# Performance work log

Hardware: AMD Instinct MI355X
Metric: run time of the kernel (lower is better)

Reference implementation:

```python
import jax, jax.numpy as jnp
import numpy as np

N = 400000
INC = 32
OUTC = 32
K = 27  # 3x3x3 kernel offsets
BN_EPS = 1e-5


def setup_inputs() -> dict:
    key = jax.random.key(0)
    ks = jax.random.split(key, 6)
    feats = jax.random.normal(ks[0], (N, INC), dtype=jnp.float32)
    kernel = jax.random.normal(ks[1], (K, INC, OUTC), dtype=jnp.float32) * 0.05
    bn_gamma = jnp.ones((OUTC,), dtype=jnp.float32)
    bn_beta = jnp.zeros((OUTC,), dtype=jnp.float32)
    bn_mean = jax.random.normal(ks[2], (OUTC,), dtype=jnp.float32) * 0.1
    bn_var = jax.random.uniform(ks[3], (OUTC,), dtype=jnp.float32) + 0.5
    in_idx = jax.random.randint(ks[4], (K, N), 0, N, dtype=jnp.int32)
    out_idx = jax.random.randint(ks[5], (K, N), 0, N, dtype=jnp.int32)
    return {"feats": feats, "kernel": kernel, "bn_gamma": bn_gamma,
            "bn_beta": bn_beta, "bn_mean": bn_mean, "bn_var": bn_var,
            "in_idx": in_idx, "out_idx": out_idx}


def _sparse_conv(feats, kernel, in_idx, out_idx):
    # gather -> per-offset matmul -> scatter-add, looped over the 27 offsets
    # via lax.scan to avoid materializing a [K, N, C] intermediate.
    out0 = jnp.zeros((feats.shape[0], kernel.shape[-1]), dtype=feats.dtype)

    def step(out, xs):
        w_k, iin, iout = xs  # [inc,outc], [M], [M]
        gathered = feats[iin]              # [M, inc]  irregular gather
        contrib = gathered @ w_k           # [M, outc] per-offset GEMM
        return out.at[iout].add(contrib), None  # scatter-accumulate

    out, _ = jax.lax.scan(step, out0, (kernel, in_idx, out_idx))
    return out


def reference(feats, kernel, bn_gamma, bn_beta, bn_mean, bn_var, in_idx, out_idx):
    out = _sparse_conv(feats, kernel, in_idx, out_idx)
    # BatchNorm (eval mode, running stats) over the feature dim
    inv_std = jax.lax.rsqrt(bn_var + BN_EPS)
    out = (out - bn_mean) * (bn_gamma * inv_std) + bn_beta
    # ReLU
    return jnp.maximum(out, 0.0)
```

## Files before the change

### kernel.cpp

```cpp
#include <hip/hip_runtime.h>
#include <hip/hip_bf16.h>
#include <hip/hip_fp16.h>

constexpr int INC  = 32;
constexpr int OUTC = 32;
constexpr int CHROWS  = 256;
constexpr int NSLICE  = 8;
constexpr int CAPB    = 384;
constexpr int CPS_MAX = 208;
constexpr int ACCW    = 17;

typedef __bf16 bf16x8 __attribute__((ext_vector_type(8)));
typedef float  f32x4  __attribute__((ext_vector_type(4)));
typedef __attribute__((address_space(3))) unsigned long long lds_u64;


__device__ __forceinline__ void lds_add_u64(unsigned long long* p,
                                            unsigned long long v) {
    __hip_atomic_fetch_add((lds_u64*)p, v,
                           __ATOMIC_RELAXED, __HIP_MEMORY_SCOPE_WORKGROUP);
}

__device__ __forceinline__ unsigned long long enc2(float a, float b) {
    const int q0 = __float2int_rn(fminf(fmaxf(a, -8.f), 8.f) * 65536.0f);
    const int q1 = __float2int_rn(fminf(fmaxf(b, -8.f), 8.f) * 65536.0f);
    return (unsigned long long)((long long)q0 + ((long long)q1 << 32));
}

__global__ __launch_bounds__(256) void prep_feats(
    const float* __restrict__ f, __bf16* __restrict__ fb, int total8)
{
    int i = blockIdx.x * 256 + threadIdx.x;
    const int stride = gridDim.x * 256;
    for (; i < total8; i += stride) {
        const float4* p = (const float4*)(f + (size_t)i * 8);
        const float4 a = p[0], b = p[1];
        bf16x8 v;
        v[0] = (__bf16)a.x; v[1] = (__bf16)a.y; v[2] = (__bf16)a.z; v[3] = (__bf16)a.w;
        v[4] = (__bf16)b.x; v[5] = (__bf16)b.y; v[6] = (__bf16)b.z; v[7] = (__bf16)b.w;
        *(bf16x8*)(fb + (size_t)i * 8) = v;
    }
}

__global__ __launch_bounds__(1024) void fill_chunks(
    const int* __restrict__ in_idx,
    const int* __restrict__ out_idx,
    unsigned* __restrict__ recsB,
    unsigned* __restrict__ cntB,
    int N, int cps, int slice_rows)
{
    __shared__ unsigned cur[CPS_MAX];
    const int s = blockIdx.x, k = blockIdx.y;
    const int tid = threadIdx.x;
    for (int c = tid; c < cps; c += 1024) cur[c] = 0u;
    __syncthreads();

    const int* iin_p  = in_idx  + (size_t)k * N;
    const int* iout_p = out_idx + (size_t)k * N;
    const int nchunkpad = NSLICE * cps;
    const unsigned lo = (unsigned)(s * slice_rows);
    const unsigned hi = lo + (unsigned)slice_rows;
    const size_t segbase = ((size_t)k * nchunkpad + (size_t)s * cps) * CAPB;

    for (int i0 = tid * 4; i0 < N; i0 += 4096) {
        const int4 ov = *(const int4*)(iout_p + i0);
        const int4 iv = *(const int4*)(iin_p + i0);
        const unsigned o[4]  = {(unsigned)ov.x, (unsigned)ov.y,
                                (unsigned)ov.z, (unsigned)ov.w};
        const unsigned ii[4] = {(unsigned)iv.x, (unsigned)iv.y,
                                (unsigned)iv.z, (unsigned)iv.w};
#pragma unroll
        for (int j = 0; j < 4; ++j) {
            if (o[j] >= lo && o[j] < hi) {
                const unsigned olo  = o[j] - lo;
                const unsigned c    = olo >> 8;
                const unsigned lrow = olo & 255u;
                const unsigned pos = atomicAdd(&cur[c], 1u);
                if (pos < (unsigned)CAPB)
                    recsB[segbase + (size_t)c * CAPB + pos] = ii[j] | (lrow << 19);
            }
        }
    }
    __syncthreads();
    for (int c = tid; c < cps; c += 1024)
        cntB[(size_t)k * nchunkpad + (size_t)s * cps + c] =
            min(cur[c], (unsigned)CAPB);
}

template<bool BF16F>
__global__ __launch_bounds__(576) void conv_chunk(
    const float*  __restrict__ feats,
    const __bf16* __restrict__ fbf,
    const float*  __restrict__ wkern,
    const unsigned* __restrict__ recsB,
    const unsigned* __restrict__ cntB,
    const float* __restrict__ gamma, const float* __restrict__ beta,
    const float* __restrict__ mean,  const float* __restrict__ var,
    float* __restrict__ out, int N, int nchunkpad)
{
    __shared__ unsigned long long accw[(CHROWS + 1) * ACCW];
    const int tid = threadIdx.x;
    for (int i = tid; i < (CHROWS + 1) * ACCW; i += 576) accw[i] = 0ull;
    __syncthreads();

    const int c    = blockIdx.x;
    const int wid  = tid >> 6;
    const int lane = tid & 63;
    const int col  = lane & 15;
    const int quad = lane >> 4;

#pragma unroll
    for (int kk = 0; kk < 3; ++kk) {
        const int k = wid + kk * 9;
        const int bidx = k * nchunkpad + c;
        const int cnt = (int)cntB[bidx];
        if (cnt == 0) continue;
        const unsigned* seg = recsB + (size_t)bidx * CAPB;

        const float* wk = wkern + (size_t)k * (INC * OUTC);
        bf16x8 b0, b1;
#pragma unroll
        for (int j = 0; j < 8; ++j) {
            const float2 w2 = *(const float2*)(wk + (quad * 8 + j) * OUTC + 2 * col);
            b0[j] = (__bf16)w2.x;
            b1[j] = (__bf16)w2.y;
        }

        const int ntile = (cnt + 15) >> 4;

        auto do_tile = [&](int t) {
            const int sbase = t << 4;
            const unsigned ra = seg[sbase + col];
            const unsigned iidx = (sbase + col < cnt) ? (ra & 0x7FFFFu) : 0u;
            bf16x8 a;
            if constexpr (BF16F) {
                a = *(const bf16x8*)(fbf + (size_t)iidx * INC + quad * 8);
            } else {
                const float4* ap = (const float4*)(feats + (size_t)iidx * INC + quad * 8);
                const float4 alo = ap[0], ahi = ap[1];
                a[0] = (__bf16)alo.x; a[1] = (__bf16)alo.y;
                a[2] = (__bf16)alo.z; a[3] = (__bf16)alo.w;
                a[4] = (__bf16)ahi.x; a[5] = (__bf16)ahi.y;
                a[6] = (__bf16)ahi.z; a[7] = (__bf16)ahi.w;
            }
            const uint4 rv = *(const uint4*)(seg + sbase + quad * 4);
            f32x4 acc0 = {0.f, 0.f, 0.f, 0.f};
            f32x4 acc1 = {0.f, 0.f, 0.f, 0.f};
            acc0 = __builtin_amdgcn_mfma_f32_16x16x32_bf16(a, b0, acc0, 0, 0, 0);
            acc1 = __builtin_amdgcn_mfma_f32_16x16x32_bf16(a, b1, acc1, 0, 0, 0);
            const unsigned rr[4] = { rv.x, rv.y, rv.z, rv.w };
#pragma unroll
            for (int r = 0; r < 4; ++r) {
                const int idx  = sbase + quad * 4 + r;
                const int lrow = (idx < cnt) ? (int)((rr[r] >> 19) & 255u) : CHROWS;
                lds_add_u64(&accw[lrow * ACCW + col], enc2(acc0[r], acc1[r]));
            }
        };

        int t = 0;
        for (; t + 2 <= ntile; t += 2) {
            const int s0 = t << 4, s1 = s0 + 16;
            const unsigned ra0 = seg[s0 + col];
            const unsigned ra1 = seg[s1 + col];
            const uint4 rv0 = *(const uint4*)(seg + s0 + quad * 4);
            const uint4 rv1 = *(const uint4*)(seg + s1 + quad * 4);
            const unsigned i0 = (s0 + col < cnt) ? (ra0 & 0x7FFFFu) : 0u;
            const unsigned i1 = (s1 + col < cnt) ? (ra1 & 0x7FFFFu) : 0u;

            bf16x8 a0, a1;
            if constexpr (BF16F) {
                a0 = *(const bf16x8*)(fbf + (size_t)i0 * INC + quad * 8);
                a1 = *(const bf16x8*)(fbf + (size_t)i1 * INC + quad * 8);
            } else {
                const float4* p0 = (const float4*)(feats + (size_t)i0 * INC + quad * 8);
                const float4* p1 = (const float4*)(feats + (size_t)i1 * INC + quad * 8);
                const float4 a0lo = p0[0], a0hi = p0[1];
                const float4 a1lo = p1[0], a1hi = p1[1];
                a0[0] = (__bf16)a0lo.x; a0[1] = (__bf16)a0lo.y;
                a0[2] = (__bf16)a0lo.z; a0[3] = (__bf16)a0lo.w;
                a0[4] = (__bf16)a0hi.x; a0[5] = (__bf16)a0hi.y;
                a0[6] = (__bf16)a0hi.z; a0[7] = (__bf16)a0hi.w;
                a1[0] = (__bf16)a1lo.x; a1[1] = (__bf16)a1lo.y;
                a1[2] = (__bf16)a1lo.z; a1[3] = (__bf16)a1lo.w;
                a1[4] = (__bf16)a1hi.x; a1[5] = (__bf16)a1hi.y;
                a1[6] = (__bf16)a1hi.z; a1[7] = (__bf16)a1hi.w;
            }

            f32x4 c00 = {0.f, 0.f, 0.f, 0.f};
            f32x4 c01 = {0.f, 0.f, 0.f, 0.f};
            f32x4 c10 = {0.f, 0.f, 0.f, 0.f};
            f32x4 c11 = {0.f, 0.f, 0.f, 0.f};
            c00 = __builtin_amdgcn_mfma_f32_16x16x32_bf16(a0, b0, c00, 0, 0, 0);
            c01 = __builtin_amdgcn_mfma_f32_16x16x32_bf16(a0, b1, c01, 0, 0, 0);
            c10 = __builtin_amdgcn_mfma_f32_16x16x32_bf16(a1, b0, c10, 0, 0, 0);
            c11 = __builtin_amdgcn_mfma_f32_16x16x32_bf16(a1, b1, c11, 0, 0, 0);

            const unsigned rr0[4] = { rv0.x, rv0.y, rv0.z, rv0.w };
            const unsigned rr1[4] = { rv1.x, rv1.y, rv1.z, rv1.w };
#pragma unroll
            for (int r = 0; r < 4; ++r) {
                const int idx0  = s0 + quad * 4 + r;
                const int lrow0 = (idx0 < cnt) ? (int)((rr0[r] >> 19) & 255u) : CHROWS;
                lds_add_u64(&accw[lrow0 * ACCW + col], enc2(c00[r], c01[r]));
            }
#pragma unroll
            for (int r = 0; r < 4; ++r) {
                const int idx1  = s1 + quad * 4 + r;
                const int lrow1 = (idx1 < cnt) ? (int)((rr1[r] >> 19) & 255u) : CHROWS;
                lds_add_u64(&accw[lrow1 * ACCW + col], enc2(c10[r], c11[r]));
            }
        }
        for (; t < ntile; ++t) do_tile(t);
    }
    __syncthreads();

    if (tid < 512) {
        const int p  = tid & 15;
        const int c0 = 2 * p;
        const int r0 = tid >> 4;
        const float s0 = gamma[c0]     * rsqrtf(var[c0]     + 1e-5f);
        const float s1 = gamma[c0 + 1] * rsqrtf(var[c0 + 1] + 1e-5f);
        const float q0 = beta[c0]     - mean[c0]     * s0;
        const float q1 = beta[c0 + 1] - mean[c0 + 1] * s1;
#pragma unroll
        for (int it = 0; it < CHROWS / 32; ++it) {
            const int row  = it * 32 + r0;
            const int grow = c * CHROWS + row;
            if (grow < N) {
                long long t = (long long)accw[row * ACCW + p];
                const int d0 = (int)(unsigned)(t & 0xFFFFFFFFll);
                const int d1 = (int)((t - (long long)d0) >> 32);
                float2 o;
                o.x = fmaxf(fmaf((float)d0 * (1.f / 65536.f), s0, q0), 0.f);
                o.y = fmaxf(fmaf((float)d1 * (1.f / 65536.f), s1, q1), 0.f);
                *(float2*)(out + (size_t)grow * OUTC + c0) = o;
            }
        }
    }
}

__global__ __launch_bounds__(256) void scatter_conv_mfma_pk(
    const float* __restrict__ feats,
    const float* __restrict__ wkern,
    const int*   __restrict__ in_idx,
    const int*   __restrict__ out_idx,
    __half2*     __restrict__ ws,
    int N)
{
    const int k    = blockIdx.y;
    const int lane = threadIdx.x & 63;
    const int col  = lane & 15;
    const int quad = lane >> 4;

    const int wave   = blockIdx.x * 4 + (threadIdx.x >> 6);
    const int nwaves = gridDim.x * 4;

    const float* wk = wkern + (size_t)k * (INC * OUTC);
    bf16x8 b0, b1;
#pragma unroll
    for (int j = 0; j < 8; ++j) {
        const int kk = quad * 8 + j;
        b0[j] = (__bf16)wk[kk * OUTC + 2 * col];
        b1[j] = (__bf16)wk[kk * OUTC + 2 * col + 1];
    }

    const int* iin_p  = in_idx  + (size_t)k * N;
    const int* iout_p = out_idx + (size_t)k * N;
    const int  ntiles = N >> 4;

    for (int t = wave; t < ntiles; t += nwaves) {
        const int base = t << 4;
        const int iin = iin_p[base + col];
        int orow[4];
#pragma unroll
        for (int r = 0; r < 4; ++r) orow[r] = iout_p[base + quad * 4 + r];

        const float4* ap = (const float4*)(feats + (size_t)iin * INC + quad * 8);
        const float4 a_lo = ap[0];
        const float4 a_hi = ap[1];
        bf16x8 a;
        a[0] = (__bf16)a_lo.x; a[1] = (__bf16)a_lo.y;
        a[2] = (__bf16)a_lo.z; a[3] = (__bf16)a_lo.w;
        a[4] = (__bf16)a_hi.x; a[5] = (__bf16)a_hi.y;
        a[6] = (__bf16)a_hi.z; a[7] = (__bf16)a_hi.w;

        f32x4 acc0 = {0.f, 0.f, 0.f, 0.f};
        f32x4 acc1 = {0.f, 0.f, 0.f, 0.f};
        acc0 = __builtin_amdgcn_mfma_f32_16x16x32_bf16(a, b0, acc0, 0, 0, 0);
        acc1 = __builtin_amdgcn_mfma_f32_16x16x32_bf16(a, b1, acc1, 0, 0, 0);

#pragma unroll
        for (int r = 0; r < 4; ++r) {
            __half2 v = __halves2half2(__float2half(acc0[r]), __float2half(acc1[r]));
            unsafeAtomicAdd(ws + (size_t)orow[r] * 16 + col, v);
        }
    }
}

__global__ __launch_bounds__(256) void bn_relu_f16(
    const __half2* __restrict__ ws,
    float* __restrict__ out,
    const float* __restrict__ gamma,
    const float* __restrict__ beta,
    const float* __restrict__ mean,
    const float* __restrict__ var,
    int total2)
{
    const int tid    = blockIdx.x * blockDim.x + threadIdx.x;
    const int stride = gridDim.x * blockDim.x;
    const int p      = tid & 15;
    const int c0     = 2 * p;

    float s0 = gamma[c0]     * rsqrtf(var[c0]     + 1e-5f);
    float s1 = gamma[c0 + 1] * rsqrtf(var[c0 + 1] + 1e-5f);
    float q0 = beta[c0]     - mean[c0]     * s0;
    float q1 = beta[c0 + 1] - mean[c0 + 1] * s1;

    float2* po = (float2*)out;
    for (int i = tid; i < total2; i += stride) {
        const __half2 h = ws[i];
        float2 v;
        v.x = fmaxf(fmaf(__low2float(h),  s0, q0), 0.0f);
        v.y = fmaxf(fmaf(__high2float(h), s1, q1), 0.0f);
        po[i] = v;
    }
}

__global__ __launch_bounds__(256) void scatter_conv_mfma_f32(
    const float* __restrict__ feats,
    const float* __restrict__ wkern,
    const int*   __restrict__ in_idx,
    const int*   __restrict__ out_idx,
    float*       __restrict__ out,
    int N)
{
    const int k    = blockIdx.y;
    const int lane = threadIdx.x & 63;
    const int col  = lane & 15;
    const int quad = lane >> 4;
    const int wave   = blockIdx.x * 4 + (threadIdx.x >> 6);
    const int nwaves = gridDim.x * 4;

    const float* wk = wkern + (size_t)k * (INC * OUTC);
    bf16x8 b0, b1;
#pragma unroll
    for (int j = 0; j < 8; ++j) {
        const int kk = quad * 8 + j;
        b0[j] = (__bf16)wk[kk * OUTC + col];
        b1[j] = (__bf16)wk[kk * OUTC + 16 + col];
    }

    const int* iin_p  = in_idx  + (size_t)k * N;
    const int* iout_p = out_idx + (size_t)k * N;
    const int  ntiles = N >> 4;

    for (int t = wave; t < ntiles; t += nwaves) {
        const int base = t << 4;
        const int iin = iin_p[base + col];
        int orow[4];
#pragma unroll
        for (int r = 0; r < 4; ++r) orow[r] = iout_p[base + quad * 4 + r];

        const float4* ap = (const float4*)(feats + (size_t)iin * INC + quad * 8);
        const float4 a_lo = ap[0];
        const float4 a_hi = ap[1];
        bf16x8 a;
        a[0] = (__bf16)a_lo.x; a[1] = (__bf16)a_lo.y;
        a[2] = (__bf16)a_lo.z; a[3] = (__bf16)a_lo.w;
        a[4] = (__bf16)a_hi.x; a[5] = (__bf16)a_hi.y;
        a[6] = (__bf16)a_hi.z; a[7] = (__bf16)a_hi.w;

        f32x4 acc0 = {0.f, 0.f, 0.f, 0.f};
        f32x4 acc1 = {0.f, 0.f, 0.f, 0.f};
        acc0 = __builtin_amdgcn_mfma_f32_16x16x32_bf16(a, b0, acc0, 0, 0, 0);
        acc1 = __builtin_amdgcn_mfma_f32_16x16x32_bf16(a, b1, acc1, 0, 0, 0);

#pragma unroll
        for (int r = 0; r < 4; ++r) {
            float* dst = out + (size_t)orow[r] * OUTC + col;
            unsafeAtomicAdd(dst,      acc0[r]);
            unsafeAtomicAdd(dst + 16, acc1[r]);
        }
    }
}

__global__ __launch_bounds__(256) void bn_relu_f32_inplace(
    float* __restrict__ out,
    const float* __restrict__ gamma,
    const float* __restrict__ beta,
    const float* __restrict__ mean,
    const float* __restrict__ var,
    int total4)
{
    const int tid    = blockIdx.x * blockDim.x + threadIdx.x;
    const int stride = gridDim.x * blockDim.x;
    const int c0     = (tid & 7) << 2;

    float s[4], b[4];
#pragma unroll
    for (int j = 0; j < 4; ++j) {
        const int c = c0 + j;
        s[j] = gamma[c] * rsqrtf(var[c] + 1e-5f);
        b[j] = beta[c] - mean[c] * s[j];
    }

    float4* p = (float4*)out;
    for (int i = tid; i < total4; i += stride) {
        float4 v = p[i];
        v.x = fmaxf(fmaf(v.x, s[0], b[0]), 0.0f);
        v.y = fmaxf(fmaf(v.y, s[1], b[1]), 0.0f);
        v.z = fmaxf(fmaf(v.z, s[2], b[2]), 0.0f);
        v.w = fmaxf(fmaf(v.w, s[3], b[3]), 0.0f);
        p[i] = v;
    }
}

extern "C" void kernel_launch(void* const* d_in, const int* in_sizes, int n_in,
                              void* d_out, int out_size, void* d_ws, size_t ws_size,
                              hipStream_t stream) {
    const float* feats   = (const float*)d_in[0];
    const float* wkern   = (const float*)d_in[1];
    const float* gamma   = (const float*)d_in[2];
    const float* beta    = (const float*)d_in[3];
    const float* mean    = (const float*)d_in[4];
    const float* var     = (const float*)d_in[5];
    const int*   in_idx  = (const int*)d_in[6];
    const int*   out_idx = (const int*)d_in[7];
    float*       out     = (float*)d_out;

    const int N = in_sizes[0] / INC;
    const int K = in_sizes[1] / (INC * OUTC);

    const int nchunk     = (N + CHROWS - 1) / CHROWS;
    const int cps        = (nchunk + NSLICE - 1) / NSLICE;
    const int nchunkpad  = NSLICE * cps;
    const int slice_rows = cps * CHROWS;

    auto al = [](size_t x) { return (x + 255) & ~(size_t)255; };
    size_t off = 0;
    const size_t cntB_off  = off; off = al(off + (size_t)K * nchunkpad * 4);
    const size_t recsB_off = off; off = al(off + (size_t)K * nchunkpad * CAPB * 4);
    const size_t need_core = off;
    const size_t fbf_off   = off;
    const size_t need_full = off + al((size_t)N * INC * 2);
    const size_t need_pk   = (size_t)N * OUTC * sizeof(__half);

    const bool chunk_ok = (N <= (1 << 19)) && (N % 4 == 0) &&
                          (cps <= CPS_MAX) && (K == 27);

    if (chunk_ok && ws_size >= need_core) {
        char* base = (char*)d_ws;
        unsigned* cntB  = (unsigned*)(base + cntB_off);
        unsigned* recsB = (unsigned*)(base + recsB_off);

        const bool use_bf16 = ws_size >= need_full;
        if (use_bf16) {
            __bf16* fbf = (__bf16*)(base + fbf_off);
            prep_feats<<<768, 256, 0, stream>>>(feats, fbf, N * 4);
            fill_chunks<<<dim3(NSLICE, K), 1024, 0, stream>>>(
                in_idx, out_idx, recsB, cntB, N, cps, slice_rows);
            conv_chunk<true><<<nchunk, 576, 0, stream>>>(
                feats, fbf, wkern, recsB, cntB, gamma, beta, mean, var,
                out, N, nchunkpad);
        } else {
            fill_chunks<<<dim3(NSLICE, K), 1024, 0, stream>>>(
                in_idx, out_idx, recsB, cntB, N, cps, slice_rows);
            conv_chunk<false><<<nchunk, 576, 0, stream>>>(
                feats, nullptr, wkern, recsB, cntB, gamma, beta, mean, var,
                out, N, nchunkpad);
        }
    } else if (ws_size >= need_pk) {
        __half2* acc = (__half2*)d_ws;
        hipMemsetAsync(acc, 0, need_pk, stream);
        dim3 grid(80, K);
        scatter_conv_mfma_pk<<<grid, 256, 0, stream>>>(
            feats, wkern, in_idx, out_idx, acc, N);
        bn_relu_f16<<<1024, 256, 0, stream>>>(acc, out, gamma, beta, mean, var, N * 16);
    } else {
        hipMemsetAsync(out, 0, (size_t)out_size * sizeof(float), stream);
        dim3 grid(80, K);
        scatter_conv_mfma_f32<<<grid, 256, 0, stream>>>(
            feats, wkern, in_idx, out_idx, out, N);
        bn_relu_f32_inplace<<<1024, 256, 0, stream>>>(
            out, gamma, beta, mean, var, out_size / 4);
    }
}
```

Measured before the change: 559.6 us.

## Partition index scan across blocks and bin records per chunk-part

```diff
diff --git a/kernel.cpp b/kernel.cpp
--- a/kernel.cpp
+++ b/kernel.cpp
@@ -4,15 +4,16 @@
 
 constexpr int INC  = 32;
 constexpr int OUTC = 32;
-constexpr int CHROWS  = 256;
-constexpr int NSLICE  = 8;
-constexpr int CAPB    = 384;
-constexpr int CPS_MAX = 208;
-constexpr int ACCW    = 17;
+constexpr int CHROWS = 256;
+constexpr int NPART  = 8;
+constexpr int CAPP   = 80;
+constexpr int NCHMAX = 2048;
+constexpr int ACCW   = 17;
 
 typedef __bf16 bf16x8 __attribute__((ext_vector_type(8)));
 typedef float  f32x4  __attribute__((ext_vector_type(4)));
 typedef __attribute__((address_space(3))) unsigned long long lds_u64;
+typedef __attribute__((address_space(3))) unsigned           lds_u32;
 
 
 __device__ __forceinline__ void lds_add_u64(unsigned long long* p,
@@ -20,10 +21,14 @@
     __hip_atomic_fetch_add((lds_u64*)p, v,
                            __ATOMIC_RELAXED, __HIP_MEMORY_SCOPE_WORKGROUP);
 }
+__device__ __forceinline__ unsigned lds_add_u32(unsigned* p, unsigned v) {
+    return __hip_atomic_fetch_add((lds_u32*)p, v,
+                                  __ATOMIC_RELAXED, __HIP_MEMORY_SCOPE_WORKGROUP);
+}
 
 __device__ __forceinline__ unsigned long long enc2(float a, float b) {
-    const int q0 = __float2int_rn(fminf(fmaxf(a, -8.f), 8.f) * 65536.0f);
-    const int q1 = __float2int_rn(fminf(fmaxf(b, -8.f), 8.f) * 65536.0f);
+    const int q0 = __float2int_rn(a * 65536.0f);
+    const int q1 = __float2int_rn(b * 65536.0f);
     return (unsigned long long)((long long)q0 + ((long long)q1 << 32));
 }
 
@@ -42,27 +47,27 @@
     }
 }
 
-__global__ __launch_bounds__(1024) void fill_chunks(
+__global__ __launch_bounds__(1024) void fill_parts(
     const int* __restrict__ in_idx,
     const int* __restrict__ out_idx,
     unsigned* __restrict__ recsB,
     unsigned* __restrict__ cntB,
-    int N, int cps, int slice_rows)
-{
-    __shared__ unsigned cur[CPS_MAX];
-    const int s = blockIdx.x, k = blockIdx.y;
+    int N, int nchunk, int nchunkpad)
+{
+    __shared__ unsigned cur[NCHMAX];
+    const int p = blockIdx.x, k = blockIdx.y;
     const int tid = threadIdx.x;
-    for (int c = tid; c < cps; c += 1024) cur[c] = 0u;
+    for (int c = tid; c < nchunk; c += 1024) cur[c] = 0u;
     __syncthreads();
 
+    const int part_n  = N / NPART;
+    const int ibeg    = p * part_n;
+    const int iend    = ibeg + part_n;
     const int* iin_p  = in_idx  + (size_t)k * N;
     const int* iout_p = out_idx + (size_t)k * N;
-    const int nchunkpad = NSLICE * cps;
-    const unsigned lo = (unsigned)(s * slice_rows);
-    const unsigned hi = lo + (unsigned)slice_rows;
-    const size_t segbase = ((size_t)k * nchunkpad + (size_t)s * cps) * CAPB;
-
-    for (int i0 = tid * 4; i0 < N; i0 += 4096) {
+    const size_t kbase8 = (size_t)k * nchunkpad * NPART;
+
+    for (int i0 = ibeg + tid * 4; i0 < iend; i0 += 4096) {
         const int4 ov = *(const int4*)(iout_p + i0);
         const int4 iv = *(const int4*)(iin_p + i0);
         const unsigned o[4]  = {(unsigned)ov.x, (unsigned)ov.y,
@@ -71,20 +76,17 @@
                                 (unsigned)iv.z, (unsigned)iv.w};
 #pragma unroll
         for (int j = 0; j < 4; ++j) {
-            if (o[j] >= lo && o[j] < hi) {
-                const unsigned olo  = o[j] - lo;
-                const unsigned c    = olo >> 8;
-                const unsigned lrow = olo & 255u;
-                const unsigned pos = atomicAdd(&cur[c], 1u);
-                if (pos < (unsigned)CAPB)
-                    recsB[segbase + (size_t)c * CAPB + pos] = ii[j] | (lrow << 19);
-            }
+            const unsigned c    = o[j] >> 8;
+            const unsigned lrow = o[j] & 255u;
+            const unsigned pos  = lds_add_u32(&cur[c], 1u);
+            if (pos < (unsigned)CAPP)
+                recsB[(kbase8 + (size_t)c * NPART + p) * CAPP + pos]
+                    = ii[j] | (lrow << 19);
         }
     }
     __syncthreads();
-    for (int c = tid; c < cps; c += 1024)
-        cntB[(size_t)k * nchunkpad + (size_t)s * cps + c] =
-            min(cur[c], (unsigned)CAPB);
+    for (int c = tid; c < nchunk; c += 1024)
+        cntB[kbase8 + (size_t)c * NPART + p] = min(cur[c], (unsigned)CAPP);
 }
 
 template<bool BF16F>
@@ -109,13 +111,10 @@
     const int col  = lane & 15;
     const int quad = lane >> 4;
 
-#pragma unroll
+#pragma unroll 1
     for (int kk = 0; kk < 3; ++kk) {
         const int k = wid + kk * 9;
-        const int bidx = k * nchunkpad + c;
-        const int cnt = (int)cntB[bidx];
-        if (cnt == 0) continue;
-        const unsigned* seg = recsB + (size_t)bidx * CAPB;
+        const size_t bidx8 = ((size_t)k * nchunkpad + c) * NPART;
 
         const float* wk = wkern + (size_t)k * (INC * OUTC);
         bf16x8 b0, b1;
@@ -126,91 +125,97 @@
             b1[j] = (__bf16)w2.y;
         }
 
-        const int ntile = (cnt + 15) >> 4;
-
-        auto do_tile = [&](int t) {
-            const int sbase = t << 4;
-            const unsigned ra = seg[sbase + col];
-            const unsigned iidx = (sbase + col < cnt) ? (ra & 0x7FFFFu) : 0u;
-            bf16x8 a;
-            if constexpr (BF16F) {
-                a = *(const bf16x8*)(fbf + (size_t)iidx * INC + quad * 8);
-            } else {
-                const float4* ap = (const float4*)(feats + (size_t)iidx * INC + quad * 8);
-                const float4 alo = ap[0], ahi = ap[1];
-                a[0] = (__bf16)alo.x; a[1] = (__bf16)alo.y;
-                a[2] = (__bf16)alo.z; a[3] = (__bf16)alo.w;
-                a[4] = (__bf16)ahi.x; a[5] = (__bf16)ahi.y;
-                a[6] = (__bf16)ahi.z; a[7] = (__bf16)ahi.w;
+#pragma unroll 1
+        for (int p = 0; p < NPART; ++p) {
+            const int cnt = (int)cntB[bidx8 + p];
+            if (cnt == 0) continue;
+            const unsigned* seg = recsB + (bidx8 + p) * CAPP;
+            const int ntile = (cnt + 15) >> 4;
+
+            auto do_tile = [&](int t) {
+                const int sbase = t << 4;
+                const unsigned ra = seg[sbase + col];
+                const unsigned iidx = (sbase + col < cnt) ? (ra & 0x7FFFFu) : 0u;
+                bf16x8 a;
+                if constexpr (BF16F) {
+                    a = *(const bf16x8*)(fbf + (size_t)iidx * INC + quad * 8);
+                } else {
+                    const float4* ap = (const float4*)(feats + (size_t)iidx * INC + quad * 8);
+                    const float4 alo = ap[0], ahi = ap[1];
+                    a[0] = (__bf16)alo.x; a[1] = (__bf16)alo.y;
+                    a[2] = (__bf16)alo.z; a[3] = (__bf16)alo.w;
+                    a[4] = (__bf16)ahi.x; a[5] = (__bf16)ahi.y;
+                    a[6] = (__bf16)ahi.z; a[7] = (__bf16)ahi.w;
+                }
+                const uint4 rv = *(const uint4*)(seg + sbase + quad * 4);
+                f32x4 acc0 = {0.f, 0.f, 0.f, 0.f};
+                f32x4 acc1 = {0.f, 0.f, 0.f, 0.f};
+                acc0 = __builtin_amdgcn_mfma_f32_16x16x32_bf16(a, b0, acc0, 0, 0, 0);
+                acc1 = __builtin_amdgcn_mfma_f32_16x16x32_bf16(a, b1, acc1, 0, 0, 0);
+                const unsigned rr[4] = { rv.x, rv.y, rv.z, rv.w };
+#pragma unroll
+                for (int r = 0; r < 4; ++r) {
+                    const int idx  = sbase + quad * 4 + r;
+                    const int lrow = (idx < cnt) ? (int)((rr[r] >> 19) & 255u) : CHROWS;
+                    lds_add_u64(&accw[lrow * ACCW + col], enc2(acc0[r], acc1[r]));
+                }
+            };
+
+            int t = 0;
+            for (; t + 2 <= ntile; t += 2) {
+                const int s0 = (t << 4), s1 = s0 + 16;
+                const unsigned ra0 = seg[s0 + col];
+                const unsigned ra1 = seg[s1 + col];
+                const uint4 rv0 = *(const uint4*)(seg + s0 + quad * 4);
+                const uint4 rv1 = *(const uint4*)(seg + s1 + quad * 4);
+                const unsigned i0 = (s0 + col < cnt) ? (ra0 & 0x7FFFFu) : 0u;
+                const unsigned i1 = (s1 + col < cnt) ? (ra1 & 0x7FFFFu) : 0u;
+
+                bf16x8 a0, a1;
+                if constexpr (BF16F) {
+                    a0 = *(const bf16x8*)(fbf + (size_t)i0 * INC + quad * 8);
+                    a1 = *(const bf16x8*)(fbf + (size_t)i1 * INC + quad * 8);
+                } else {
+                    const float4* p0 = (const float4*)(feats + (size_t)i0 * INC + quad * 8);
+                    const float4* p1 = (const float4*)(feats + (size_t)i1 * INC + quad * 8);
+                    const float4 a0lo = p0[0], a0hi = p0[1];
+                    const float4 a1lo = p1[0], a1hi = p1[1];
+                    a0[0] = (__bf16)a0lo.x; a0[1] = (__bf16)a0lo.y;
+                    a0[2] = (__bf16)a0lo.z; a0[3] = (__bf16)a0lo.w;
+                    a0[4] = (__bf16)a0hi.x; a0[5] = (__bf16)a0hi.y;
+                    a0[6] = (__bf16)a0hi.z; a0[7] = (__bf16)a0hi.w;
+                    a1[0] = (__bf16)a1lo.x; a1[1] = (__bf16)a1lo.y;
+                    a1[2] = (__bf16)a1lo.z; a1[3] = (__bf16)a1lo.w;
+                    a1[4] = (__bf16)a1hi.x; a1[5] = (__bf16)a1hi.y;
+                    a1[6] = (__bf16)a1hi.z; a1[7] = (__bf16)a1hi.w;
+                }
+
+                f32x4 c00 = {0.f, 0.f, 0.f, 0.f};
+                f32x4 c01 = {0.f, 0.f, 0.f, 0.f};
+                f32x4 c10 = {0.f, 0.f, 0.f, 0.f};
+                f32x4 c11 = {0.f, 0.f, 0.f, 0.f};
+                c00 = __builtin_amdgcn_mfma_f32_16x16x32_bf16(a0, b0, c00, 0, 0, 0);
+                c01 = __builtin_amdgcn_mfma_f32_16x16x32_bf16(a0, b1, c01, 0, 0, 0);
+                c10 = __builtin_amdgcn_mfma_f32_16x16x32_bf16(a1, b0, c10, 0, 0, 0);
+                c11 = __builtin_amdgcn_mfma_f32_16x16x32_bf16(a1, b1, c11, 0, 0, 0);
+
+                const unsigned rr0[4] = { rv0.x, rv0.y, rv0.z, rv0.w };
+                const unsigned rr1[4] = { rv1.x, rv1.y, rv1.z, rv1.w };
+#pragma unroll
+                for (int r = 0; r < 4; ++r) {
+                    const int idx0  = s0 + quad * 4 + r;
+                    const int lrow0 = (idx0 < cnt) ? (int)((rr0[r] >> 19) & 255u) : CHROWS;
+                    lds_add_u64(&accw[lrow0 * ACCW + col], enc2(c00[r], c01[r]));
+                }
+#pragma unroll
+                for (int r = 0; r < 4; ++r) {
+                    const int idx1  = s1 + quad * 4 + r;
+                    const int lrow1 = (idx1 < cnt) ? (int)((rr1[r] >> 19) & 255u) : CHROWS;
+                    lds_add_u64(&accw[lrow1 * ACCW + col], enc2(c10[r], c11[r]));
+                }
             }
-            const uint4 rv = *(const uint4*)(seg + sbase + quad * 4);
-            f32x4 acc0 = {0.f, 0.f, 0.f, 0.f};
-            f32x4 acc1 = {0.f, 0.f, 0.f, 0.f};
-            acc0 = __builtin_amdgcn_mfma_f32_16x16x32_bf16(a, b0, acc0, 0, 0, 0);
-            acc1 = __builtin_amdgcn_mfma_f32_16x16x32_bf16(a, b1, acc1, 0, 0, 0);
-            const unsigned rr[4] = { rv.x, rv.y, rv.z, rv.w };
-#pragma unroll
-            for (int r = 0; r < 4; ++r) {
-                const int idx  = sbase + quad * 4 + r;
-                const int lrow = (idx < cnt) ? (int)((rr[r] >> 19) & 255u) : CHROWS;
-                lds_add_u64(&accw[lrow * ACCW + col], enc2(acc0[r], acc1[r]));
-            }
-        };
-
-        int t = 0;
-        for (; t + 2 <= ntile; t += 2) {
-            const int s0 = t << 4, s1 = s0 + 16;
-            const unsigned ra0 = seg[s0 + col];
-            const unsigned ra1 = seg[s1 + col];
-            const uint4 rv0 = *(const uint4*)(seg + s0 + quad * 4);
-            const uint4 rv1 = *(const uint4*)(seg + s1 + quad * 4);
-            const unsigned i0 = (s0 + col < cnt) ? (ra0 & 0x7FFFFu) : 0u;
-            const unsigned i1 = (s1 + col < cnt) ? (ra1 & 0x7FFFFu) : 0u;
-
-            bf16x8 a0, a1;
-            if constexpr (BF16F) {
-                a0 = *(const bf16x8*)(fbf + (size_t)i0 * INC + quad * 8);
-                a1 = *(const bf16x8*)(fbf + (size_t)i1 * INC + quad * 8);
-            } else {
-                const float4* p0 = (const float4*)(feats + (size_t)i0 * INC + quad * 8);
-                const float4* p1 = (const float4*)(feats + (size_t)i1 * INC + quad * 8);
-                const float4 a0lo = p0[0], a0hi = p0[1];
-                const float4 a1lo = p1[0], a1hi = p1[1];
-                a0[0] = (__bf16)a0lo.x; a0[1] = (__bf16)a0lo.y;
-                a0[2] = (__bf16)a0lo.z; a0[3] = (__bf16)a0lo.w;
-                a0[4] = (__bf16)a0hi.x; a0[5] = (__bf16)a0hi.y;
-                a0[6] = (__bf16)a0hi.z; a0[7] = (__bf16)a0hi.w;
-                a1[0] = (__bf16)a1lo.x; a1[1] = (__bf16)a1lo.y;
-                a1[2] = (__bf16)a1lo.z; a1[3] = (__bf16)a1lo.w;
-                a1[4] = (__bf16)a1hi.x; a1[5] = (__bf16)a1hi.y;
-                a1[6] = (__bf16)a1hi.z; a1[7] = (__bf16)a1hi.w;
-            }
-
-            f32x4 c00 = {0.f, 0.f, 0.f, 0.f};
-            f32x4 c01 = {0.f, 0.f, 0.f, 0.f};
-            f32x4 c10 = {0.f, 0.f, 0.f, 0.f};
-            f32x4 c11 = {0.f, 0.f, 0.f, 0.f};
-            c00 = __builtin_amdgcn_mfma_f32_16x16x32_bf16(a0, b0, c00, 0, 0, 0);
-            c01 = __builtin_amdgcn_mfma_f32_16x16x32_bf16(a0, b1, c01, 0, 0, 0);
-            c10 = __builtin_amdgcn_mfma_f32_16x16x32_bf16(a1, b0, c10, 0, 0, 0);
-            c11 = __builtin_amdgcn_mfma_f32_16x16x32_bf16(a1, b1, c11, 0, 0, 0);
-
-            const unsigned rr0[4] = { rv0.x, rv0.y, rv0.z, rv0.w };
-            const unsigned rr1[4] = { rv1.x, rv1.y, rv1.z, rv1.w };
-#pragma unroll
-            for (int r = 0; r < 4; ++r) {
-                const int idx0  = s0 + quad * 4 + r;
-                const int lrow0 = (idx0 < cnt) ? (int)((rr0[r] >> 19) & 255u) : CHROWS;
-                lds_add_u64(&accw[lrow0 * ACCW + col], enc2(c00[r], c01[r]));
-            }
-#pragma unroll
-            for (int r = 0; r < 4; ++r) {
-                const int idx1  = s1 + quad * 4 + r;
-                const int lrow1 = (idx1 < cnt) ? (int)((rr1[r] >> 19) & 255u) : CHROWS;
-                lds_add_u64(&accw[lrow1 * ACCW + col], enc2(c10[r], c11[r]));
-            }
-        }
-        for (; t < ntile; ++t) do_tile(t);
+            for (; t < ntile; ++t) do_tile(t);
+        }
     }
     __syncthreads();
 
@@ -431,22 +436,22 @@
     const int N = in_sizes[0] / INC;
     const int K = in_sizes[1] / (INC * OUTC);
 
-    const int nchunk     = (N + CHROWS - 1) / CHROWS;
-    const int cps        = (nchunk + NSLICE - 1) / NSLICE;
-    const int nchunkpad  = NSLICE * cps;
-    const int slice_rows = cps * CHROWS;
+    const int nchunk    = (N + CHROWS - 1) / CHROWS;
+    const int nchunkpad = (nchunk + 31) & ~31;
 
     auto al = [](size_t x) { return (x + 255) & ~(size_t)255; };
     size_t off = 0;
-    const size_t cntB_off  = off; off = al(off + (size_t)K * nchunkpad * 4);
-    const size_t recsB_off = off; off = al(off + (size_t)K * nchunkpad * CAPB * 4);
+    const size_t cntB_off  = off;
+    off = al(off + (size_t)K * nchunkpad * NPART * 4);
+    const size_t recsB_off = off;
+    off = al(off + (size_t)K * nchunkpad * NPART * CAPP * 4);
     const size_t need_core = off;
     const size_t fbf_off   = off;
     const size_t need_full = off + al((size_t)N * INC * 2);
     const size_t need_pk   = (size_t)N * OUTC * sizeof(__half);
 
-    const bool chunk_ok = (N <= (1 << 19)) && (N % 4 == 0) &&
-                          (cps <= CPS_MAX) && (K == 27);
+    const bool chunk_ok = (N <= (1 << 19)) && (N % (NPART * 4) == 0) &&
+                          (nchunk <= NCHMAX) && (K == 27);
 
     if (chunk_ok && ws_size >= need_core) {
         char* base = (char*)d_ws;
@@ -457,14 +462,14 @@
         if (use_bf16) {
             __bf16* fbf = (__bf16*)(base + fbf_off);
             prep_feats<<<768, 256, 0, stream>>>(feats, fbf, N * 4);
-            fill_chunks<<<dim3(NSLICE, K), 1024, 0, stream>>>(
-                in_idx, out_idx, recsB, cntB, N, cps, slice_rows);
+            fill_parts<<<dim3(NPART, K), 1024, 0, stream>>>(
+                in_idx, out_idx, recsB, cntB, N, nchunk, nchunkpad);
             conv_chunk<true><<<nchunk, 576, 0, stream>>>(
                 feats, fbf, wkern, recsB, cntB, gamma, beta, mean, var,
                 out, N, nchunkpad);
         } else {
-            fill_chunks<<<dim3(NSLICE, K), 1024, 0, stream>>>(
-                in_idx, out_idx, recsB, cntB, N, cps, slice_rows);
+            fill_parts<<<dim3(NPART, K), 1024, 0, stream>>>(
+                in_idx, out_idx, recsB, cntB, N, nchunk, nchunkpad);
             conv_chunk<false><<<nchunk, 576, 0, stream>>>(
                 feats, nullptr, wkern, recsB, cntB, gamma, beta, mean, var,
                 out, N, nchunkpad);
```

New measurement: 644.7 us. +15.2%, slower.
